# Performance work log

Hardware: AMD Instinct MI355X
Metric: run time of the kernel (lower is better)

Reference implementation:

```python
import jax, jax.numpy as jnp
from jax import lax
import numpy as np

NUM_HEADS = 4
EPS = 1e-5


def refl_conv(x, W, stride):
    # ReflectionPad2d(1) + Conv2d(k=3, bias=False), NCHW/OIHW
    x = jnp.pad(x, ((0, 0), (0, 0), (1, 1), (1, 1)), mode='reflect')
    return lax.conv_general_dilated(x, W, (stride, stride), 'VALID',
                                    dimension_numbers=('NCHW', 'OIHW', 'NCHW'))


def instance_norm(x):
    # nn.InstanceNorm2d (affine=False, biased var, eps=1e-5)
    m = jnp.mean(x, axis=(2, 3), keepdims=True)
    v = jnp.var(x, axis=(2, 3), keepdims=True)
    return (x - m) * lax.rsqrt(v + EPS)


def iln(x, rho, gamma, beta):
    # UGATIT Instance-Layer Norm; torch.var default is unbiased (ddof=1)
    in_m = jnp.mean(x, axis=(2, 3), keepdims=True)
    in_v = jnp.var(x, axis=(2, 3), keepdims=True, ddof=1)
    ln_m = jnp.mean(x, axis=(1, 2, 3), keepdims=True)
    ln_v = jnp.var(x, axis=(1, 2, 3), keepdims=True, ddof=1)
    out = rho * (x - in_m) * lax.rsqrt(in_v + EPS) \
        + (1.0 - rho) * (x - ln_m) * lax.rsqrt(ln_v + EPS)
    return out * gamma + beta


def upsample2(x):
    # nn.Upsample(scale_factor=2, mode='nearest')
    return jnp.repeat(jnp.repeat(x, 2, axis=2), 2, axis=3)


def pos_encoding(x):
    # sin/cos positional encoding over flattened HW, added per channel
    b, c, h, w = x.shape
    half = c // 2
    pos = jnp.arange(h * w, dtype=x.dtype)                  # [L]
    depths = jnp.arange(half, dtype=x.dtype) / half          # [c/2]
    rates = 1.0 / (10000.0 ** depths)
    ang = pos[:, None] * rates[None, :]                      # [L, c/2]
    pe = jnp.concatenate([jnp.sin(ang), jnp.cos(ang)], axis=-1)  # [L, c]
    return (x.reshape(b, c, h * w) + pe.T[None]).reshape(b, c, h, w)


def mha(q, k, v, num_heads):
    # q,k,v: [b, n, c]; hand-rolled QK^T-softmax-V (dropout=0)
    b, n, c = q.shape
    d = c // num_heads
    split = lambda t: t.reshape(b, t.shape[1], num_heads, d).transpose(0, 2, 1, 3)
    qh, kh, vh = split(q), split(k), split(v)                # [b, h, n, d]
    scores = jnp.einsum('bhid,bhjd->bhij', qh, kh) * (d ** -0.5)
    attn = jax.nn.softmax(scores, axis=-1)                   # full NxN materialized
    out = jnp.einsum('bhij,bhjd->bhid', attn, vh)
    return out.transpose(0, 2, 1, 3).reshape(b, n, c)


def setup_inputs() -> dict:
    key = jax.random.key(0)
    ks = jax.random.split(key, 8)
    W = 0.05
    return {
        'y': jax.random.normal(ks[0], (2, 256, 64, 64), jnp.float32),
        's': jax.random.normal(ks[1], (2, 128, 128, 128), jnp.float32),
        'w_blue_s': jax.random.normal(ks[2], (128, 128, 3, 3), jnp.float32) * W,
        'w_blue_y': jax.random.normal(ks[3], (128, 256, 3, 3), jnp.float32) * W,
        'w_purple': jax.random.normal(ks[4], (128, 128, 3, 3), jnp.float32) * W,
        'rho_p': jax.random.uniform(ks[5], (1, 128, 1, 1), jnp.float32),
        'gamma_p': jnp.ones((1, 128, 1, 1), jnp.float32),
        'beta_p': jnp.zeros((1, 128, 1, 1), jnp.float32),
        'w_green': jax.random.normal(ks[6], (128, 256, 3, 3), jnp.float32) * W,
        'rho_g': jax.random.uniform(ks[7], (1, 128, 1, 1), jnp.float32),
        'gamma_g': jnp.ones((1, 128, 1, 1), jnp.float32),
        'beta_g': jnp.zeros((1, 128, 1, 1), jnp.float32),
    }


def reference(y, s, w_blue_s, w_blue_y, w_purple, rho_p, gamma_p, beta_p,
              w_green, rho_g, gamma_g, beta_g):
    b, yc, yh, yw = y.shape
    sc = yc // 2
    # green_y: upsample -> refl conv -> ILN -> SiLU
    up_y = jax.nn.silu(iln(refl_conv(upsample2(y), w_green, 1), rho_g, gamma_g, beta_g))
    y_pe = pos_encoding(y)
    s_pe = pos_encoding(s)
    # blue_y (stride 1) -> q = k; blue_s (stride 2) -> v
    q2d = jax.nn.silu(instance_norm(refl_conv(y_pe, w_blue_y, 1)))   # [b, sc, yh, yw]
    v2d = jax.nn.silu(instance_norm(refl_conv(s_pe, w_blue_s, 2)))   # [b, sc, yh, yw]
    q = q2d.reshape(b, sc, yh * yw).transpose(0, 2, 1)               # [b, N, sc]
    v = v2d.reshape(b, sc, -1).transpose(0, 2, 1)
    out = mha(q, q, v, NUM_HEADS)                                     # [b, N, sc]
    mha2d = out.transpose(0, 2, 1).reshape(b, sc, yh, yw)
    # purple: upsample -> refl conv -> ILN -> sigmoid; gate s
    z = jax.nn.sigmoid(iln(refl_conv(upsample2(mha2d), w_purple, 1),
                           rho_p, gamma_p, beta_p)) * s
    return jnp.concatenate([z, up_y], axis=1)                         # [b, yc, 2yh, 2yw]
```

## Files before the change

kernel.cpp:

```cpp
#include <hip/hip_runtime.h>
#include <math.h>

#define EPS 1e-5f

typedef __attribute__((ext_vector_type(8))) _Float16 f16x8;
typedef __attribute__((ext_vector_type(4))) float f32x4;
typedef __attribute__((ext_vector_type(2))) __fp16 fp16x2;

union H8u { ushort4 u[2]; uint4 q; f16x8 h; };
union PKu { fp16x2 h; unsigned int u; };

__device__ __forceinline__ float sigmoidf_(float x){ return 1.f/(1.f+__expf(-x)); }

__device__ __forceinline__ unsigned short f2h(float f){
  union { _Float16 h; unsigned short u; } c;
  c.h = (_Float16)f;
  return c.u;
}

__device__ __forceinline__ void block_reduce2(float& s, float& s2){
  __shared__ float ls[16], ls2[16];
  #pragma unroll
  for (int off = 32; off; off >>= 1){
    s  += __shfl_down(s, off);
    s2 += __shfl_down(s2, off);
  }
  int wid = threadIdx.x >> 6, lane = threadIdx.x & 63;
  int nw = blockDim.x >> 6;
  if (lane == 0){ ls[wid] = s; ls2[wid] = s2; }
  __syncthreads();
  if (threadIdx.x == 0){
    float a = ls[0], b = ls2[0];
    for (int i = 1; i < nw; i++){ a += ls[i]; b += ls2[i]; }
    ls[0] = a; ls2[0] = b;
  }
  __syncthreads();
  s = ls[0]; s2 = ls2[0];
}

__global__ __launch_bounds__(256) void pe_t_kernel(
    const float* __restrict__ x, unsigned short* __restrict__ xt,
    unsigned short* __restrict__ xt2,
    int C, int L, int half, int addpe){
  __shared__ unsigned short tile[64][72];
  __shared__ unsigned short tile2[64][72];
  int b = blockIdx.z;
  int c0 = blockIdx.y * 64, l0 = blockIdx.x * 64;
  int tid = threadIdx.x;
  const float l2r = 13.28771237954945f;
  #pragma unroll
  for (int i = 0; i < 4; i++){
    int id = tid + i * 256;
    int c = id >> 4, ch = (id & 15) * 4;
    int cg = c0 + c;
    float4 v = *(const float4*)&x[((long)b * C + cg) * L + l0 + ch];
    float pe0 = 0.f, pe1 = 0.f, pe2 = 0.f, pe3 = 0.f;
    if (addpe){
      int d = cg < half ? cg : cg - half;
      float rate = exp2f(-l2r * (float)d / (float)half);
      float a0 = (float)(l0 + ch) * rate;
      if (cg < half){ pe0 = sinf(a0); pe1 = sinf(a0 + rate); pe2 = sinf(a0 + 2.f*rate); pe3 = sinf(a0 + 3.f*rate); }
      else          { pe0 = cosf(a0); pe1 = cosf(a0 + rate); pe2 = cosf(a0 + 2.f*rate); pe3 = cosf(a0 + 3.f*rate); }
    }
    ushort4 o;
    o.x = f2h(v.x + pe0); o.y = f2h(v.y + pe1);
    o.z = f2h(v.z + pe2); o.w = f2h(v.w + pe3);
    *(ushort4*)&tile[c][ch] = o;
    if (xt2){
      ushort4 o2;
      o2.x = f2h(v.x); o2.y = f2h(v.y); o2.z = f2h(v.z); o2.w = f2h(v.w);
      *(ushort4*)&tile2[c][ch] = o2;
    }
  }
  __syncthreads();
  #pragma unroll
  for (int i = 0; i < 2; i++){
    int id = tid + i * 256;
    int l = id >> 3, ch = (id & 7) * 8;
    ushort4 a, bq;
    a.x = tile[ch+0][l]; a.y = tile[ch+1][l]; a.z = tile[ch+2][l]; a.w = tile[ch+3][l];
    bq.x = tile[ch+4][l]; bq.y = tile[ch+5][l]; bq.z = tile[ch+6][l]; bq.w = tile[ch+7][l];
    unsigned short* op = &xt[((long)b * L + l0 + l) * C + c0 + ch];
    *(ushort4*)op = a;
    *(ushort4*)(op + 4) = bq;
    if (xt2){
      ushort4 a2, b2;
      a2.x = tile2[ch+0][l]; a2.y = tile2[ch+1][l]; a2.z = tile2[ch+2][l]; a2.w = tile2[ch+3][l];
      b2.x = tile2[ch+4][l]; b2.y = tile2[ch+5][l]; b2.z = tile2[ch+6][l]; b2.w = tile2[ch+7][l];
      unsigned short* op2 = &xt2[((long)b * L + l0 + l) * C + c0 + ch];
      *(ushort4*)op2 = a2;
      *(ushort4*)(op2 + 4) = b2;
    }
  }
}

__device__ __forceinline__ unsigned short wffP_elem(const float* __restrict__ w, int Cin, int idx){
  int NCH = Cin >> 5;
  int per_tap = NCH << 9;
  int e = idx & 7, lane = (idx >> 3) & 63, chunk = (idx >> 9) % NCH;
  int tap = (idx / per_tap) % 9, coB = idx / (9 * per_tap);
  int lg = lane >> 4, lr = lane & 15;
  int co = coB * 16 + lr;
  int ch = chunk * 32 + ((e < 4) ? lg * 4 + e : 16 + lg * 4 + e - 4);
  return f2h(w[((long)co * Cin + ch) * 9 + tap]);
}

__device__ __forceinline__ unsigned short wffF_elem(const float* __restrict__ w, int Cin, int idx){
  int NCH = Cin >> 5;
  int per_tap = NCH << 9;
  int per_p = 8 * 4 * per_tap;
  int e = idx & 7, lane = (idx >> 3) & 63, chunk = (idx >> 9) % NCH;
  int tap = (idx / per_tap) % 4;
  int coB = (idx / (4 * per_tap)) % 8;
  int p = idx / per_p;
  int ph = p >> 1, pw = p & 1, kr = tap >> 1, kc = tap & 1;
  int lg = lane >> 4, lr = lane & 15;
  int co = coB * 16 + lr;
  int ch = chunk * 32 + ((e < 4) ? lg * 4 + e : 16 + lg * 4 + e - 4);
  const float* wb = &w[((long)co * Cin + ch) * 9];
  float sum = 0.f;
  for (int kh = 0; kh < 3; kh++){
    bool rok = (ph == 0) ? (kr == 0 ? kh == 0 : kh >= 1)
                         : (kr == 0 ? kh <= 1 : kh == 2);
    if (!rok) continue;
    for (int kw = 0; kw < 3; kw++){
      bool cok = (pw == 0) ? (kc == 0 ? kw == 0 : kw >= 1)
                           : (kc == 0 ? kw <= 1 : kw == 2);
      if (cok) sum += wb[kh * 3 + kw];
    }
  }
  return f2h(sum);
}

__global__ __launch_bounds__(256) void wprep_all_kernel(
    const float* __restrict__ wby, const float* __restrict__ wbs,
    const float* __restrict__ wg,  const float* __restrict__ wp,
    unsigned short* __restrict__ oby, unsigned short* __restrict__ obs,
    unsigned short* __restrict__ og,  unsigned short* __restrict__ op){
  const int T0 = 294912, T1 = T0 + 147456, T2 = T1 + 524288, T3 = T2 + 262144;
  for (int idx = blockIdx.x * blockDim.x + threadIdx.x; idx < T3;
       idx += gridDim.x * blockDim.x){
    if (idx < T0)       oby[idx]      = wffP_elem(wby, 256, idx);
    else if (idx < T1)  obs[idx - T0] = wffP_elem(wbs, 128, idx - T0);
    else if (idx < T2)  og[idx - T1]  = wffF_elem(wg, 256, idx - T1);
    else                op[idx - T2]  = wffF_elem(wp, 128, idx - T2);
  }
}

template<int NTAP, int CSHIFT, int UP>
__global__ __launch_bounds__(256) void conv_tile_kernel(
    const unsigned short* __restrict__ xt, const unsigned short* __restrict__ wff,
    unsigned short* __restrict__ out,
    int Hin, int Win, int stride, int Wout, int woutLog, int HWout){
  constexpr int Cin = 8 << CSHIFT;
  constexpr int NCHUNK = 1 << (CSHIFT - 2);
  __shared__ __align__(16) char stage[NCHUNK * 4112];
  __shared__ int rowIdx[NTAP][64];
  int tid = threadIdx.x;
  int lane = tid & 63, wid = tid >> 6;
  int lg = lane >> 4, lr = lane & 15;
  int b, par = 0;
  if (UP){ par = blockIdx.z & 3; b = blockIdx.z >> 2; } else b = blockIdx.z;
  const unsigned short* xb = xt + (long)b * Hin * Win * Cin;
  int coB = blockIdx.y * 4 + wid;

  if (UP){
    int ph = par >> 1, pw = par & 1;
    int ii = blockIdx.x;
    int VH = 2 * Hin, VW = 2 * Win;
    for (int id = tid; id < NTAP * 64; id += 256){
      int tap = id >> 6, r = id & 63;
      int kr = tap >> 1, kc = tap & 1;
      int v = 2 * ii + (ph == 0 ? (kr == 0 ? -1 : 0) : (kr == 0 ? 0 : 2));
      v = v < 0 ? -v : (v >= VH ? 2 * VH - 2 - v : v);
      int u = 2 * r + (pw == 0 ? (kc == 0 ? -1 : 0) : (kc == 0 ? 0 : 2));
      u = u < 0 ? -u : (u >= VW ? 2 * VW - 2 - u : u);
      rowIdx[tap][r] = (v >> 1) * Win + (u >> 1);
    }
  } else {
    int sp0 = blockIdx.x * 64;
    for (int id = tid; id < NTAP * 64; id += 256){
      int tap = id >> 6, r = id & 63;
      int kh = tap / 3, kw = tap - kh * 3;
      int sp = sp0 + r;
      int oh = sp >> woutLog, ow = sp & (Wout - 1);
      int ih = oh * stride - 1 + kh;
      ih = ih < 0 ? -ih : (ih >= Hin ? 2 * Hin - 2 - ih : ih);
      int iw = ow * stride - 1 + kw;
      iw = iw < 0 ? -iw : (iw >= Win ? 2 * Win - 2 - iw : iw);
      rowIdx[tap][r] = ih * Win + iw;
    }
  }

  f32x4 acc[4];
  #pragma unroll
  for (int f = 0; f < 4; f++) acc[f] = (f32x4){0.f, 0.f, 0.f, 0.f};

  const unsigned short* wbase =
      wff + ((long)((UP ? par : 0) * 8 + coB) * NTAP) * (NCHUNK * 512) + lane * 8;

  for (int tap = 0; tap < NTAP; tap++){
    __syncthreads();
    #pragma unroll
    for (int i2 = 0; i2 < NCHUNK; i2++){
      int id = tid + (i2 << 8);
      int sp = id >> CSHIFT;
      int c8 = (id & ((1 << CSHIFT) - 1)) << 3;
      int chunk = c8 >> 5, c = c8 & 31;
      int lgb = (c & 15) >> 2, hoff = (c >> 4) & 1;
      uint4 g = *(const uint4*)&xb[(long)rowIdx[tap][sp] * Cin + c8];
      int slot = ((chunk * 4 + (sp >> 4)) * 64 + lgb * 16 + (sp & 15)) * 16
                 + hoff * 8 + chunk * 16;
      *(uint2*)(stage + slot)       = make_uint2(g.x, g.y);
      *(uint2*)(stage + slot + 256) = make_uint2(g.z, g.w);
    }
    __syncthreads();
    const unsigned short* wp = wbase + (long)tap * (NCHUNK * 512);
    #pragma unroll
    for (int ch = 0; ch < NCHUNK; ch++){
      H8u A; A.q = *(const uint4*)(wp + ch * 512);
      #pragma unroll
      for (int f = 0; f < 4; f++){
        H8u X; X.q = *(const uint4*)(stage + ((ch * 4 + f) * 64 + lane) * 16 + ch * 16);
        acc[f] = __builtin_amdgcn_mfma_f32_16x16x32_f16(A.h, X.h, acc[f], 0, 0, 0);
      }
    }
  }

  unsigned short* ob = out + (long)b * 128 * HWout;
  #pragma unroll
  for (int f = 0; f < 4; f++){
    int spl = f * 16 + lr;
    long opos;
    if (UP){
      int oh = 2 * blockIdx.x + (par >> 1);
      int ow = 2 * spl + (par & 1);
      opos = (long)oh * Wout + ow;
    } else opos = (long)blockIdx.x * 64 + spl;
    #pragma unroll
    for (int r = 0; r < 4; r++){
      int co = coB * 16 + lg * 4 + r;
      ob[(long)co * HWout + opos] = f2h(acc[f][r]);
    }
  }
}

__global__ __launch_bounds__(256) void in_silu2_kernel(
    const unsigned short* __restrict__ qx, unsigned short* __restrict__ outT,
    const unsigned short* __restrict__ vx, unsigned short* __restrict__ outV, int HW){
  int which = blockIdx.y;
  int bc = blockIdx.x;
  const unsigned short* p = (which ? vx : qx) + (long)bc * HW;
  int i0 = threadIdx.x * 16;
  H8u a, b2;
  a.q  = *(const uint4*)&p[i0];
  b2.q = *(const uint4*)&p[i0 + 8];
  float v[16];
  float s = 0.f, s2 = 0.f;
  #pragma unroll
  for (int j = 0; j < 8; j++){ v[j] = (float)a.h[j]; v[8+j] = (float)b2.h[j]; }
  #pragma unroll
  for (int j = 0; j < 16; j++){ s += v[j]; s2 += v[j]*v[j]; }
  block_reduce2(s, s2);
  float mean = s / (float)HW;
  float var  = s2 / (float)HW - mean * mean;
  float rstd = rsqrtf(var + EPS);
  if (which == 0){
    int b = bc >> 7, cg = bc & 127, h = cg >> 5, d = cg & 31;
    unsigned short* op = outT + ((long)(b * 4 + h) * HW) * 32 + d;
    #pragma unroll
    for (int j = 0; j < 16; j++){
      float t = (v[j] - mean) * rstd;
      t = t * sigmoidf_(t);
      op[(long)(i0 + j) * 32] = f2h(t);
    }
  } else {
    H8u o0, o1;
    #pragma unroll
    for (int j = 0; j < 8; j++){
      float t = (v[j] - mean) * rstd;
      o0.h[j] = (_Float16)(t * sigmoidf_(t));
      float t1 = (v[8+j] - mean) * rstd;
      o1.h[j] = (_Float16)(t1 * sigmoidf_(t1));
    }
    unsigned short* op = outV + (long)bc * HW + i0;
    *(uint4*)op = o0.q;
    *(uint4*)(op + 8) = o1.q;
  }
}

__global__ __launch_bounds__(1024, 8) void flash_attn_kernel(
    const unsigned short* __restrict__ qk,
    const unsigned short* __restrict__ vt,
    unsigned short* __restrict__ mhaT, int N){
  __shared__ float smem[16384];
  unsigned short* sstage = (unsigned short*)smem;
  const float SCALE2 = 0.25503257066404493f;

  int bh = blockIdx.y;
  int b = bh >> 2, h = bh & 3;
  int tid = threadIdx.x;
  int ks = tid >> 8;
  int t256 = tid & 255;
  int qg = (tid >> 6) & 3;
  int lane = tid & 63;
  int lg = lane >> 4, lr = lane & 15;
  const unsigned short* qbase = qk + (long)bh * N * 32;
  const unsigned short* vbase = vt + (long)(b * 128 + h * 32) * N;
  int ksu = ks * 4096;

  int q0w = blockIdx.x * 64 + qg * 16;
  f16x8 qf;
  {
    const unsigned short* qp = qbase + (long)(q0w + lr) * 32 + lg * 4;
    H8u Q;
    Q.u[0] = *(const ushort4*)qp;
    Q.u[1] = *(const ushort4*)(qp + 16);
    qf = Q.h;
    const _Float16 sc = (_Float16)SCALE2;
    #pragma unroll
    for (int j = 0; j < 8; j++) qf[j] = qf[j] * sc;
  }

  int skey = t256 >> 2, sq4 = t256 & 3;
  int kdst = ksu + (((skey >> 4) * 4 + (sq4 & 1) * 2) * 16 + (skey & 15)) * 8 + (sq4 >> 1) * 4;
  int sd = t256 >> 3, soct = t256 & 7;
  int vx = (soct >> 2) * 2 + (soct & 1);
  int vdst = ksu + 2048 +
      ((((soct >> 2) * 2 + (sd >> 4)) * 4 + (soct & 1) * 2) * 16 + ((sd & 15) ^ vx)) * 8 +
      ((soct >> 1) & 1) * 4;

  float m_run = -1e30f, l_run = 0.f;
  f32x4 acc0 = {0.f,0.f,0.f,0.f}, acc1 = {0.f,0.f,0.f,0.f};

  const int NT = N >> 8;

  {
    int k0 = ks * NT * 64;
    uint4 kl = *(const uint4*)(qbase + (long)(k0 + skey) * 32 + sq4 * 8);
    *(uint2*)(&sstage[kdst])       = make_uint2(kl.x, kl.y);
    *(uint2*)(&sstage[kdst + 128]) = make_uint2(kl.z, kl.w);
    uint4 vl = *(const uint4*)(vbase + (long)sd * N + k0 + soct * 8);
    *(uint2*)(&sstage[vdst])       = make_uint2(vl.x, vl.y);
    *(uint2*)(&sstage[vdst + 128]) = make_uint2(vl.z, vl.w);
  }
  __syncthreads();

  for (int t = 0; t < NT; t++){
    int bufc = (t & 1) << 14;
    int bufn = ((t + 1) & 1) << 14;
    uint4 kl, vl;
    bool have_next = (t + 1 < NT);
    if (have_next){
      int k0n = (ks * NT + t + 1) * 64;
      kl = *(const uint4*)(qbase + (long)(k0n + skey) * 32 + sq4 * 8);
      vl = *(const uint4*)(vbase + (long)sd * N + k0n + soct * 8);
    }

    f32x4 st[4];
    #pragma unroll
    for (int kb = 0; kb < 4; kb++){
      H8u K;
      K.q = *(const uint4*)(&sstage[bufc + ksu + (kb * 64 + lane) * 8]);
      st[kb] = __builtin_amdgcn_mfma_f32_16x16x32_f16(K.h, qf,
                  (f32x4){0.f,0.f,0.f,0.f}, 0, 0, 0);
    }

    float mk0 = fmaxf(fmaxf(fmaxf(st[0][0], st[0][1]), st[0][2]), st[0][3]);
    float mk1 = fmaxf(fmaxf(fmaxf(st[1][0], st[1][1]), st[1][2]), st[1][3]);
    float mk2 = fmaxf(fmaxf(fmaxf(st[2][0], st[2][1]), st[2][2]), st[2][3]);
    float mk3 = fmaxf(fmaxf(fmaxf(st[3][0], st[3][1]), st[3][2]), st[3][3]);
    float mt = fmaxf(fmaxf(fmaxf(mk0, mk1), mk2), mk3);
    mt = fmaxf(mt, __shfl_xor(mt, 16));
    mt = fmaxf(mt, __shfl_xor(mt, 32));

    bool noresc = __all(mt <= m_run + 8.f);
    float m_new = noresc ? m_run : fmaxf(m_run, mt);

    float lt = 0.f;
    unsigned int pup[8];
    #pragma unroll
    for (int kb = 0; kb < 4; kb++)
      #pragma unroll
      for (int rp = 0; rp < 2; rp++){
        float p0 = __builtin_amdgcn_exp2f(st[kb][2*rp]   - m_new);
        float p1 = __builtin_amdgcn_exp2f(st[kb][2*rp+1] - m_new);
        lt += p0 + p1;
        PKu pk;
        pk.h = __builtin_amdgcn_cvt_pkrtz(p0, p1);
        pup[kb * 2 + rp] = pk.u;
      }
    lt += __shfl_xor(lt, 16);
    lt += __shfl_xor(lt, 32);

    if (noresc){
      l_run += lt;
    } else {
      float fscale = __builtin_amdgcn_exp2f(m_run - m_new);
      l_run = l_run * fscale + lt;
      float fr[4];
      #pragma unroll
      for (int r = 0; r < 4; r++) fr[r] = __shfl(fscale, lg * 4 + r);
      #pragma unroll
      for (int r = 0; r < 4; r++){ acc0[r] *= fr[r]; acc1[r] *= fr[r]; }
      m_run = m_new;
    }

    #pragma unroll
    for (int m = 0; m < 2; m++){
      int xr = m * 2 + (lg >> 1);
      int laneV = lg * 16 + (lr ^ xr);
      H8u P, V0, V1;
      P.q = make_uint4(pup[4*m], pup[4*m+1], pup[4*m+2], pup[4*m+3]);
      V0.q = *(const uint4*)(&sstage[bufc + ksu + 2048 + ((m * 2 + 0) * 64 + laneV) * 8]);
      V1.q = *(const uint4*)(&sstage[bufc + ksu + 2048 + ((m * 2 + 1) * 64 + laneV) * 8]);
      acc0 = __builtin_amdgcn_mfma_f32_16x16x32_f16(P.h, V0.h, acc0, 0, 0, 0);
      acc1 = __builtin_amdgcn_mfma_f32_16x16x32_f16(P.h, V1.h, acc1, 0, 0, 0);
    }

    if (have_next){
      *(uint2*)(&sstage[bufn + kdst])       = make_uint2(kl.x, kl.y);
      *(uint2*)(&sstage[bufn + kdst + 128]) = make_uint2(kl.z, kl.w);
      *(uint2*)(&sstage[bufn + vdst])       = make_uint2(vl.x, vl.y);
      *(uint2*)(&sstage[bufn + vdst + 128]) = make_uint2(vl.z, vl.w);
    }
    __syncthreads();
  }

  float* accM = smem;
  float* mM   = smem + 8448;
  float* lM   = smem + 8704;
  #pragma unroll
  for (int r = 0; r < 4; r++){
    accM[((qg * 4 + ks) * 16 + (lg * 4 + r)) * 33 + lr]      = acc0[r];
    accM[((qg * 4 + ks) * 16 + (lg * 4 + r)) * 33 + 16 + lr] = acc1[r];
  }
  if (lg == 0){
    mM[(qg * 4 + ks) * 16 + lr] = m_run;
    lM[(qg * 4 + ks) * 16 + lr] = l_run;
  }
  __syncthreads();
  if (ks == 0){
    int q = lane >> 2, dc = lane & 3;
    float ms[4], es[4];
    float m = -1e30f;
    #pragma unroll
    for (int s = 0; s < 4; s++){ ms[s] = mM[(qg * 4 + s) * 16 + q]; m = fmaxf(m, ms[s]); }
    float l = 0.f;
    #pragma unroll
    for (int s = 0; s < 4; s++){
      es[s] = __builtin_amdgcn_exp2f(ms[s] - m);
      l += lM[(qg * 4 + s) * 16 + q] * es[s];
    }
    float inv = 1.f / l;
    float o[8];
    #pragma unroll
    for (int j = 0; j < 8; j++) o[j] = 0.f;
    #pragma unroll
    for (int s = 0; s < 4; s++){
      const float* ap = &accM[((qg * 4 + s) * 16 + q) * 33 + dc * 8];
      #pragma unroll
      for (int j = 0; j < 8; j++) o[j] += ap[j] * es[s];
    }
    ushort4 o0, o1;
    o0.x = f2h(o[0]*inv); o0.y = f2h(o[1]*inv); o0.z = f2h(o[2]*inv); o0.w = f2h(o[3]*inv);
    o1.x = f2h(o[4]*inv); o1.y = f2h(o[5]*inv); o1.z = f2h(o[6]*inv); o1.w = f2h(o[7]*inv);
    unsigned short* op = &mhaT[((long)b * N + q0w + q) * 128 + h * 32 + dc * 8];
    *(ushort4*)op = o0;
    *(ushort4*)(op + 4) = o1;
  }
}

__global__ __launch_bounds__(256) void stats2_kernel(
    const unsigned short* __restrict__ g, const unsigned short* __restrict__ p,
    float* __restrict__ statsbase, int HW){
  int which = blockIdx.y;
  long bc = blockIdx.x;
  const unsigned short* x = (which ? p : g) + bc * HW;
  float s = 0.f, s2 = 0.f;
  for (int i = threadIdx.x * 8; i < HW; i += 256 * 8){
    H8u a; a.q = *(const uint4*)&x[i];
    #pragma unroll
    for (int j = 0; j < 8; j++){ float f = (float)a.h[j]; s += f; s2 += f * f; }
  }
  block_reduce2(s, s2);
  if (threadIdx.x == 0){
    float* sums = statsbase + which * 512;
    sums[bc] = s;
    sums[256 + bc] = s2;
  }
}

__global__ __launch_bounds__(256) void iln_finalize2_kernel(
    const unsigned short* __restrict__ xg, const unsigned short* __restrict__ xp,
    const float* __restrict__ statsbase,
    const float* __restrict__ rho_p, const float* __restrict__ gamma_p,
    const float* __restrict__ beta_p,
    const float* __restrict__ rho_g, const float* __restrict__ gamma_g,
    const float* __restrict__ beta_g,
    const float* __restrict__ gate,
    float* __restrict__ out,
    int HW, int C){
  int zp = blockIdx.z;
  int bc = blockIdx.y;
  int b = bc / C, c = bc % C;
  const float* sums   = statsbase + (zp ? 0 : 512);
  const float* sumsqs = sums + 256;

  float s = 0.f, s2 = 0.f;
  if (threadIdx.x < 128){
    int cc = b * C + threadIdx.x;
    s = sums[cc]; s2 = sumsqs[cc];
  }
  block_reduce2(s, s2);
  float lsum = s, lsumsq = s2;

  float n = (float)HW;
  float im = sums[bc] / n;
  float iv = (sumsqs[bc] / n - im * im) * (n / (n - 1.f));
  float ir = rsqrtf(iv + EPS);
  float n2 = n * (float)C;
  float lm = lsum / n2;
  float lv = (lsumsq / n2 - lm * lm) * (n2 / (n2 - 1.f));
  float lr = rsqrtf(lv + EPS);
  float r  = zp ? rho_g[c]   : rho_p[c];
  float g  = zp ? gamma_g[c] : gamma_p[c];
  float bb = zp ? beta_g[c]  : beta_p[c];

  const unsigned short* xp_ = (zp ? xg : xp) + (long)bc * HW;
  const float* gp = zp ? nullptr : (gate + (long)bc * HW);
  float* op = out + ((long)(b * 256 + (zp ? 128 : 0) + c)) * HW;
  int i0 = (blockIdx.x * 256 + threadIdx.x) * 8;
  H8u a; a.q = *(const uint4*)&xp_[i0];
  float4 o0, o1;
  float res[8];
  #pragma unroll
  for (int j = 0; j < 8; j++){
    float xv = (float)a.h[j];
    float t = r * (xv - im) * ir + (1.f - r) * (xv - lm) * lr;
    t = t * g + bb;
    float sg = sigmoidf_(t);
    res[j] = zp ? t * sg : sg;
  }
  if (!zp){
    float4 g0 = *(const float4*)&gp[i0];
    float4 g1 = *(const float4*)&gp[i0 + 4];
    res[0] *= g0.x; res[1] *= g0.y; res[2] *= g0.z; res[3] *= g0.w;
    res[4] *= g1.x; res[5] *= g1.y; res[6] *= g1.z; res[7] *= g1.w;
  }
  o0.x = res[0]; o0.y = res[1]; o0.z = res[2]; o0.w = res[3];
  o1.x = res[4]; o1.y = res[5]; o1.z = res[6]; o1.w = res[7];
  *(float4*)&op[i0] = o0;
  *(float4*)&op[i0 + 4] = o1;
}

extern "C" void kernel_launch(void* const* d_in, const int* in_sizes, int n_in,
                              void* d_out, int out_size, void* d_ws, size_t ws_size,
                              hipStream_t stream){
  const float* y        = (const float*)d_in[0];
  const float* s        = (const float*)d_in[1];
  const float* w_blue_s = (const float*)d_in[2];
  const float* w_blue_y = (const float*)d_in[3];
  const float* w_purple = (const float*)d_in[4];
  const float* rho_p    = (const float*)d_in[5];
  const float* gamma_p  = (const float*)d_in[6];
  const float* beta_p   = (const float*)d_in[7];
  const float* w_green  = (const float*)d_in[8];
  const float* rho_g    = (const float*)d_in[9];
  const float* gamma_g  = (const float*)d_in[10];
  const float* beta_g   = (const float*)d_in[11];
  float* out = (float*)d_out;
  float* ws  = (float*)d_ws;

  const int B = 2, SC = 128, N = 4096, NS = 16384;

  unsigned short* s_peT = (unsigned short*)ws;
  unsigned short* y_peT = (unsigned short*)(ws + 2097152);
  unsigned short* yT    = (unsigned short*)(ws + 3145728);
  unsigned short* purple_h = (unsigned short*)ws;
  unsigned short* qbuf_h = (unsigned short*)(ws + 4194304);
  unsigned short* vbuf_h = (unsigned short*)(ws + 4718592);
  unsigned short* mhaT   = (unsigned short*)(ws + 5242880);
  unsigned short* qk_bf  = (unsigned short*)(ws + 5767168);
  unsigned short* v_bf   = (unsigned short*)(ws + 6291456);
  unsigned short* green_h = (unsigned short*)(ws + 6815744);
  unsigned short* wffP_blues = (unsigned short*)(ws + 8912896);
  unsigned short* wffP_bluey = (unsigned short*)(ws + 8986624);
  unsigned short* wffF_green = (unsigned short*)(ws + 9134080);
  unsigned short* wffF_purple = (unsigned short*)(ws + 9396224);
  float* stats = ws + 9527296;

  dim3 blk(256);

  wprep_all_kernel<<<dim3(1200), blk, 0, stream>>>(
      w_blue_y, w_blue_s, w_green, w_purple,
      wffP_bluey, wffP_blues, wffF_green, wffF_purple);

  pe_t_kernel<<<dim3(64, 4, B), blk, 0, stream>>>(y, y_peT, yT, 256, N, 128, 1);
  pe_t_kernel<<<dim3(256, 2, B), blk, 0, stream>>>(s, s_peT, nullptr, 128, NS, 64, 1);

  conv_tile_kernel<9,5,0><<<dim3(64, 2, B), blk, 0, stream>>>(
      y_peT, wffP_bluey, qbuf_h, 64, 64, 1, 64, 6, 4096);
  conv_tile_kernel<9,4,0><<<dim3(64, 2, B), blk, 0, stream>>>(
      s_peT, wffP_blues, vbuf_h, 128, 128, 2, 64, 6, 4096);

  in_silu2_kernel<<<dim3(B * SC, 2), blk, 0, stream>>>(qbuf_h, qk_bf, vbuf_h, v_bf, N);

  flash_attn_kernel<<<dim3(N / 64, B * 4), dim3(1024), 0, stream>>>(qk_bf, v_bf, mhaT, N);

  conv_tile_kernel<4,5,1><<<dim3(64, 2, B * 4), blk, 0, stream>>>(
      yT, wffF_green, green_h, 64, 64, 1, 128, 7, 16384);

  conv_tile_kernel<4,4,1><<<dim3(64, 2, B * 4), blk, 0, stream>>>(
      mhaT, wffF_purple, purple_h, 64, 64, 1, 128, 7, 16384);

  stats2_kernel<<<dim3(B * SC, 2), blk, 0, stream>>>(green_h, purple_h, stats, NS);

  iln_finalize2_kernel<<<dim3(8, B * SC, 2), blk, 0, stream>>>(
      green_h, purple_h, stats,
      rho_p, gamma_p, beta_p, rho_g, gamma_g, beta_g,
      s, out, NS, SC);
}
```

Before: 144.9 us.

## Fuse ILN partial stats into upsample convs and merge positional-encoding kernels

The upsampled green and purple conv kernels now compute per-strip partial sums and sums of squares of their fp16-rounded outputs and write them to a workspace. A small reduction kernel then combines these partials into the per-channel stats. This replaces the stats kernel that re-read both full fp16 conv outputs from memory. The two positional-encoding transpose launches are also merged into one launch that dispatches on block index, saving one launch.

```diff
diff --git a/kernel.cpp b/kernel.cpp
--- a/kernel.cpp
+++ b/kernel.cpp
@@ -38,14 +38,25 @@
   s = ls[0]; s2 = ls2[0];
 }
 
-__global__ __launch_bounds__(256) void pe_t_kernel(
-    const float* __restrict__ x, unsigned short* __restrict__ xt,
-    unsigned short* __restrict__ xt2,
-    int C, int L, int half, int addpe){
+__global__ __launch_bounds__(256) void pe_all_kernel(
+    const float* __restrict__ y, const float* __restrict__ s,
+    unsigned short* __restrict__ y_peT, unsigned short* __restrict__ yT,
+    unsigned short* __restrict__ s_peT){
   __shared__ unsigned short tile[64][72];
   __shared__ unsigned short tile2[64][72];
-  int b = blockIdx.z;
-  int c0 = blockIdx.y * 64, l0 = blockIdx.x * 64;
+  int bid = blockIdx.x;
+  const float* x; unsigned short *xt, *xt2;
+  int C, L, half, bx, by, bz;
+  if (bid < 512){
+    x = y; xt = y_peT; xt2 = yT; C = 256; L = 4096; half = 128;
+    bx = bid & 63; by = (bid >> 6) & 3; bz = bid >> 8;
+  } else {
+    int b2 = bid - 512;
+    x = s; xt = s_peT; xt2 = nullptr; C = 128; L = 16384; half = 64;
+    bx = b2 & 255; by = (b2 >> 8) & 1; bz = b2 >> 9;
+  }
+  int c0 = by * 64, l0 = bx * 64;
+  int b = bz;
   int tid = threadIdx.x;
   const float l2r = 13.28771237954945f;
   #pragma unroll
@@ -54,14 +65,12 @@
     int c = id >> 4, ch = (id & 15) * 4;
     int cg = c0 + c;
     float4 v = *(const float4*)&x[((long)b * C + cg) * L + l0 + ch];
-    float pe0 = 0.f, pe1 = 0.f, pe2 = 0.f, pe3 = 0.f;
-    if (addpe){
-      int d = cg < half ? cg : cg - half;
-      float rate = exp2f(-l2r * (float)d / (float)half);
-      float a0 = (float)(l0 + ch) * rate;
-      if (cg < half){ pe0 = sinf(a0); pe1 = sinf(a0 + rate); pe2 = sinf(a0 + 2.f*rate); pe3 = sinf(a0 + 3.f*rate); }
-      else          { pe0 = cosf(a0); pe1 = cosf(a0 + rate); pe2 = cosf(a0 + 2.f*rate); pe3 = cosf(a0 + 3.f*rate); }
-    }
+    int d = cg < half ? cg : cg - half;
+    float rate = exp2f(-l2r * (float)d / (float)half);
+    float a0 = (float)(l0 + ch) * rate;
+    float pe0, pe1, pe2, pe3;
+    if (cg < half){ pe0 = sinf(a0); pe1 = sinf(a0 + rate); pe2 = sinf(a0 + 2.f*rate); pe3 = sinf(a0 + 3.f*rate); }
+    else          { pe0 = cosf(a0); pe1 = cosf(a0 + rate); pe2 = cosf(a0 + 2.f*rate); pe3 = cosf(a0 + 3.f*rate); }
     ushort4 o;
     o.x = f2h(v.x + pe0); o.y = f2h(v.y + pe1);
     o.z = f2h(v.z + pe2); o.w = f2h(v.w + pe3);
@@ -147,10 +156,11 @@
   }
 }
 
-template<int NTAP, int CSHIFT, int UP>
+template<int NTAP, int CSHIFT, int UP, int STATS>
 __global__ __launch_bounds__(256) void conv_tile_kernel(
     const unsigned short* __restrict__ xt, const unsigned short* __restrict__ wff,
     unsigned short* __restrict__ out,
+    float* __restrict__ psum, float* __restrict__ psq, int which,
     int Hin, int Win, int stride, int Wout, int woutLog, int HWout){
   constexpr int Cin = 8 << CSHIFT;
   constexpr int NCHUNK = 1 << (CSHIFT - 2);
@@ -243,6 +253,37 @@
       ob[(long)co * HWout + opos] = f2h(acc[f][r]);
     }
   }
+
+  if constexpr (STATS){
+    float ts[4], tq[4];
+    #pragma unroll
+    for (int r = 0; r < 4; r++){ ts[r] = 0.f; tq[r] = 0.f; }
+    #pragma unroll
+    for (int f = 0; f < 4; f++)
+      #pragma unroll
+      for (int r = 0; r < 4; r++){
+        float hv = (float)(_Float16)acc[f][r];
+        ts[r] += hv; tq[r] += hv * hv;
+      }
+    #pragma unroll
+    for (int off = 1; off < 16; off <<= 1){
+      #pragma unroll
+      for (int r = 0; r < 4; r++){
+        ts[r] += __shfl_xor(ts[r], off);
+        tq[r] += __shfl_xor(tq[r], off);
+      }
+    }
+    if (lr == 0){
+      int strip = blockIdx.x * 4 + par;
+      #pragma unroll
+      for (int r = 0; r < 4; r++){
+        int co = coB * 16 + lg * 4 + r;
+        long pidx = (((long)which * 2 + b) * 128 + co) * 256 + strip;
+        psum[pidx] = ts[r];
+        psq[pidx]  = tq[r];
+      }
+    }
+  }
 }
 
 __global__ __launch_bounds__(256) void in_silu2_kernel(
@@ -471,19 +512,20 @@
   }
 }
 
-__global__ __launch_bounds__(256) void stats2_kernel(
-    const unsigned short* __restrict__ g, const unsigned short* __restrict__ p,
-    float* __restrict__ statsbase, int HW){
-  int which = blockIdx.y;
-  long bc = blockIdx.x;
-  const unsigned short* x = (which ? p : g) + bc * HW;
+__global__ __launch_bounds__(64) void stats3_kernel(
+    const float* __restrict__ psum, const float* __restrict__ psq,
+    float* __restrict__ statsbase){
+  int blockch = blockIdx.x;
+  int which = blockch >> 8, bc = blockch & 255;
+  const float* ps = psum + (long)blockch * 256;
+  const float* pq = psq  + (long)blockch * 256;
   float s = 0.f, s2 = 0.f;
-  for (int i = threadIdx.x * 8; i < HW; i += 256 * 8){
-    H8u a; a.q = *(const uint4*)&x[i];
-    #pragma unroll
-    for (int j = 0; j < 8; j++){ float f = (float)a.h[j]; s += f; s2 += f * f; }
-  }
-  block_reduce2(s, s2);
+  for (int i = threadIdx.x; i < 256; i += 64){ s += ps[i]; s2 += pq[i]; }
+  #pragma unroll
+  for (int off = 32; off; off >>= 1){
+    s  += __shfl_down(s, off);
+    s2 += __shfl_down(s2, off);
+  }
   if (threadIdx.x == 0){
     float* sums = statsbase + which * 512;
     sums[bc] = s;
@@ -589,6 +631,8 @@
   unsigned short* wffF_green = (unsigned short*)(ws + 9134080);
   unsigned short* wffF_purple = (unsigned short*)(ws + 9396224);
   float* stats = ws + 9527296;
+  float* psum  = ws + 9528320;
+  float* psq   = ws + 9659392;
 
   dim3 blk(256);
 
@@ -596,25 +640,24 @@
       w_blue_y, w_blue_s, w_green, w_purple,
       wffP_bluey, wffP_blues, wffF_green, wffF_purple);
 
-  pe_t_kernel<<<dim3(64, 4, B), blk, 0, stream>>>(y, y_peT, yT, 256, N, 128, 1);
-  pe_t_kernel<<<dim3(256, 2, B), blk, 0, stream>>>(s, s_peT, nullptr, 128, NS, 64, 1);
-
-  conv_tile_kernel<9,5,0><<<dim3(64, 2, B), blk, 0, stream>>>(
-      y_peT, wffP_bluey, qbuf_h, 64, 64, 1, 64, 6, 4096);
-  conv_tile_kernel<9,4,0><<<dim3(64, 2, B), blk, 0, stream>>>(
-      s_peT, wffP_blues, vbuf_h, 128, 128, 2, 64, 6, 4096);
+  pe_all_kernel<<<dim3(1536), blk, 0, stream>>>(y, s, y_peT, yT, s_peT);
+
+  conv_tile_kernel<9,5,0,0><<<dim3(64, 2, B), blk, 0, stream>>>(
+      y_peT, wffP_bluey, qbuf_h, nullptr, nullptr, 0, 64, 64, 1, 64, 6, 4096);
+  conv_tile_kernel<9,4,0,0><<<dim3(64, 2, B), blk, 0, stream>>>(
+      s_peT, wffP_blues, vbuf_h, nullptr, nullptr, 0, 128, 128, 2, 64, 6, 4096);
 
   in_silu2_kernel<<<dim3(B * SC, 2), blk, 0, stream>>>(qbuf_h, qk_bf, vbuf_h, v_bf, N);
 
   flash_attn_kernel<<<dim3(N / 64, B * 4), dim3(1024), 0, stream>>>(qk_bf, v_bf, mhaT, N);
 
-  conv_tile_kernel<4,5,1><<<dim3(64, 2, B * 4), blk, 0, stream>>>(
-      yT, wffF_green, green_h, 64, 64, 1, 128, 7, 16384);
-
-  conv_tile_kernel<4,4,1><<<dim3(64, 2, B * 4), blk, 0, stream>>>(
-      mhaT, wffF_purple, purple_h, 64, 64, 1, 128, 7, 16384);
-
-  stats2_kernel<<<dim3(B * SC, 2), blk, 0, stream>>>(green_h, purple_h, stats, NS);
+  conv_tile_kernel<4,5,1,1><<<dim3(64, 2, B * 4), blk, 0, stream>>>(
+      yT, wffF_green, green_h, psum, psq, 0, 64, 64, 1, 128, 7, 16384);
+
+  conv_tile_kernel<4,4,1,1><<<dim3(64, 2, B * 4), blk, 0, stream>>>(
+      mhaT, wffF_purple, purple_h, psum, psq, 1, 64, 64, 1, 128, 7, 16384);
+
+  stats3_kernel<<<dim3(512), dim3(64), 0, stream>>>(psum, psq, stats);
 
   iln_finalize2_kernel<<<dim3(8, B * SC, 2), blk, 0, stream>>>(
       green_h, purple_h, stats,
```

New measurement: 141.9 us. 2.0% less time.
